# Performance work log

Hardware: AMD Instinct MI355X
Metric: run time of the kernel (lower is better)

The kernel has to match this reference:

```python
import jax, jax.numpy as jnp
import numpy as np

H = 256
NUM_LAYERS = 3
EPS = 1e-5


def _batchnorm(x, g, b):
    # training-mode BN over axis 0 (biased variance, as torch)
    m = x.mean(axis=0)
    v = x.var(axis=0)
    return (x - m) * jax.lax.rsqrt(v + EPS) * g + b


def _layernorm(x, g, b):
    m = x.mean(axis=-1, keepdims=True)
    v = x.var(axis=-1, keepdims=True)
    return (x - m) * jax.lax.rsqrt(v + EPS) * g + b


def setup_inputs() -> dict:
    key = jax.random.key(0)
    ks = iter(jax.random.split(key, 40))
    B, N = 8, 256
    s = 0.05
    inp = {
        "node_features": jax.random.normal(next(ks), (B, N, 6), jnp.float32),
        "edge_features": jax.random.normal(next(ks), (B, N, N, 15), jnp.float32),
        "temporal_features": jax.random.normal(next(ks), (B, N, N, 4), jnp.float32),
        "adjacency": jax.random.randint(next(ks), (N, N), 0, 2, jnp.int32),
        # node embedding + BN
        "emb_W": jax.random.normal(next(ks), (H, 6), jnp.float32) * s,
        "emb_b": jnp.zeros((H,), jnp.float32),
        "node_bn_g": jnp.ones((H,), jnp.float32),
        "node_bn_b": jnp.zeros((H,), jnp.float32),
        # message passing layers (stacked over layers)
        "msg_W": jax.random.normal(next(ks), (NUM_LAYERS, H, H + 3), jnp.float32) * s,
        "msg_b": jnp.zeros((NUM_LAYERS, H), jnp.float32),
        "upd_W": jax.random.normal(next(ks), (NUM_LAYERS, H, 2 * H), jnp.float32) * s,
        "upd_b": jnp.zeros((NUM_LAYERS, H), jnp.float32),
        "bn_g": jnp.ones((NUM_LAYERS, H), jnp.float32),
        "bn_b": jnp.zeros((NUM_LAYERS, H), jnp.float32),
        # flow predictor: 2H+3+4 -> 128 -> 64 -> 1
        "fp_W1": jax.random.normal(next(ks), (128, 2 * H + 7), jnp.float32) * s,
        "fp_b1": jnp.zeros((128,), jnp.float32),
        "fp_ln1_g": jnp.ones((128,), jnp.float32),
        "fp_ln1_b": jnp.zeros((128,), jnp.float32),
        "fp_W2": jax.random.normal(next(ks), (64, 128), jnp.float32) * s,
        "fp_b2": jnp.zeros((64,), jnp.float32),
        "fp_ln2_g": jnp.ones((64,), jnp.float32),
        "fp_ln2_b": jnp.zeros((64,), jnp.float32),
        "fp_W3": jax.random.normal(next(ks), (1, 64), jnp.float32) * s,
        "fp_b3": jnp.zeros((1,), jnp.float32),
    }
    return inp


def reference(node_features, edge_features, temporal_features, adjacency,
              emb_W, emb_b, node_bn_g, node_bn_b,
              msg_W, msg_b, upd_W, upd_b, bn_g, bn_b,
              fp_W1, fp_b1, fp_ln1_g, fp_ln1_b,
              fp_W2, fp_b2, fp_ln2_g, fp_ln2_b, fp_W3, fp_b3):
    B, N = node_features.shape[0], node_features.shape[1]
    # node embedding + BN + relu (dropout = identity at eval)
    emb = node_features @ emb_W.T + emb_b  # [B,N,H]
    emb = _batchnorm(emb.reshape(-1, H), node_bn_g, node_bn_b).reshape(B, N, H)
    emb = jax.nn.relu(emb)

    er = edge_features[..., -3:]  # [B,N,N,3], indexed er[:, i, j]
    maskf = (adjacency > 0).astype(emb.dtype)  # mask[j,i]: i is neighbor of j
    deg = maskf.sum(axis=1)  # [N]

    for l in range(NUM_LAYERS):
        Wn = msg_W[l][:, :H]   # [H,H] acting on source node embedding
        We = msg_W[l][:, H:]   # [H,3] acting on edge relation
        # messages[b,j] = sum_i mask[j,i] * (emb[b,i]@Wn.T + er[b,i,j]@We.T + b)
        m1 = jnp.einsum('ji,bio->bjo', maskf, emb @ Wn.T)
        er_sum = jnp.einsum('ji,bijk->bjk', maskf, er)  # [B,N,3]
        m2 = er_sum @ We.T
        messages = m1 + m2 + deg[None, :, None] * msg_b[l]
        upd_in = jnp.concatenate([emb, messages], axis=-1)  # [B,N,2H]
        updated = jax.nn.relu(upd_in @ upd_W[l].T + upd_b[l])
        updated = _batchnorm(updated.reshape(-1, H), bn_g[l], bn_b[l]).reshape(B, N, H)
        emb = updated + emb

    # flow predictor over all (i,j) pairs, input = [emb_i, emb_j, er_ij, t_ij]
    W1i = fp_W1[:, :H]
    W1j = fp_W1[:, H:2 * H]
    W1e = fp_W1[:, 2 * H:2 * H + 3]
    W1t = fp_W1[:, 2 * H + 3:]
    h = ((emb @ W1i.T)[:, :, None, :] + (emb @ W1j.T)[:, None, :, :]
         + er @ W1e.T + temporal_features @ W1t.T + fp_b1)  # [B,N,N,128]
    h = jax.nn.relu(_layernorm(h, fp_ln1_g, fp_ln1_b))
    h = jax.nn.relu(_layernorm(h @ fp_W2.T + fp_b2, fp_ln2_g, fp_ln2_b))  # [B,N,N,64]
    flows = jax.nn.relu((h @ fp_W3.T + fp_b3)[..., 0])  # [B,N,N]
    return flows
```

## Files before the change

### kernel.cpp

```cpp
#include <hip/hip_runtime.h>

#define NB 8
#define NN 256
#define HH 256
#define RR 2048
#define EPSV 1e-5f

typedef __attribute__((ext_vector_type(8))) short short8v;
typedef __attribute__((ext_vector_type(4))) float f32x4;

static __device__ __forceinline__ short f2bf(float f){
    unsigned u = __float_as_uint(f);
    unsigned r = (u + 0x7FFFu + ((u >> 16) & 1u)) >> 16;
    return (short)r;
}

static __device__ __forceinline__ float dpp_red16(float v){
    int t;
    t = __builtin_amdgcn_update_dpp(0, __float_as_int(v), 0xB1, 0xF, 0xF, true);
    v += __int_as_float(t);
    t = __builtin_amdgcn_update_dpp(0, __float_as_int(v), 0x4E, 0xF, 0xF, true);
    v += __int_as_float(t);
    t = __builtin_amdgcn_update_dpp(0, __float_as_int(v), 0x141, 0xF, 0xF, true);
    v += __int_as_float(t);
    t = __builtin_amdgcn_update_dpp(0, __float_as_int(v), 0x140, 0xF, 0xF, true);
    v += __int_as_float(t);
    return v;
}

__global__ __launch_bounds__(256) void k_emb(const float* __restrict__ nodef,
    const float* __restrict__ embW, const float* __restrict__ embb, float* __restrict__ out)
{
    int r = blockIdx.x, c = threadIdx.x;
    const float* nr = nodef + r*6;
    const float* w  = embW + c*6;
    float acc = embb[c];
    #pragma unroll
    for(int k=0;k<6;k++) acc += nr[k]*w[k];
    out[r*HH + c] = acc;
}

__global__ __launch_bounds__(256) void k_bnstat_partial(const float* __restrict__ x, float* __restrict__ part)
{
    int g = blockIdx.x, c = threadIdx.x;
    float s=0.f, q=0.f;
    #pragma unroll
    for(int rr=0; rr<32; rr++){
        float v = x[(g*32+rr)*HH + c];
        s += v; q += v*v;
    }
    part[g*512 + c]       = s;
    part[g*512 + 256 + c] = q;
}

__global__ __launch_bounds__(256) void k_bnstat_final(const float* __restrict__ part,
    const float* __restrict__ gam, const float* __restrict__ bet,
    float* __restrict__ scale, float* __restrict__ shift)
{
    int c = threadIdx.x;
    float s=0.f, q=0.f;
    for(int g=0; g<64; g++){ s += part[g*512+c]; q += part[g*512+256+c]; }
    float m  = s * (1.f/RR);
    float v  = q * (1.f/RR) - m*m;
    float sc = gam[c] * rsqrtf(v + EPSV);
    scale[c] = sc;
    shift[c] = bet[c] - m*sc;
}

__global__ __launch_bounds__(256) void k_bnapply_relu(const float* __restrict__ x,
    const float* __restrict__ scale, const float* __restrict__ shift, float* __restrict__ emb)
{
    int e = blockIdx.x*256 + threadIdx.x;
    int c = threadIdx.x;
    float v = x[e]*scale[c] + shift[c];
    emb[e] = v > 0.f ? v : 0.f;
}

__global__ __launch_bounds__(256) void k_bnapply_res(const float* __restrict__ x,
    const float* __restrict__ scale, const float* __restrict__ shift, float* __restrict__ emb)
{
    int e = blockIdx.x*256 + threadIdx.x;
    int c = threadIdx.x;
    emb[e] += x[e]*scale[c] + shift[c];
}

__global__ __launch_bounds__(256) void k_ersum_deg(const int* __restrict__ adj,
    const float* __restrict__ ef, float* __restrict__ ersum, float* __restrict__ degv)
{
    __shared__ float sd[4][256];
    int bid = blockIdx.x;
    int b = bid >> 8, j = bid & 255;
    int i = threadIdx.x;
    float mf = adj[j*NN + i] > 0 ? 1.f : 0.f;
    int base = ((b*NN + i)*NN + j)*15 + 12;
    sd[0][i] = mf * ef[base+0];
    sd[1][i] = mf * ef[base+1];
    sd[2][i] = mf * ef[base+2];
    sd[3][i] = mf;
    __syncthreads();
    for(int s=128; s>0; s>>=1){
        if(i < s){
            sd[0][i]+=sd[0][i+s]; sd[1][i]+=sd[1][i+s];
            sd[2][i]+=sd[2][i+s]; sd[3][i]+=sd[3][i+s];
        }
        __syncthreads();
    }
    if(i==0){
        ersum[(b*NN+j)*3+0] = sd[0][0];
        ersum[(b*NN+j)*3+1] = sd[1][0];
        ersum[(b*NN+j)*3+2] = sd[2][0];
        if(b==0) degv[j] = sd[3][0];
    }
}

__global__ __launch_bounds__(256) void k_mm(const float* __restrict__ A1, const float* __restrict__ A2,
    const float* __restrict__ W, int K, int ldw, int woff,
    const float* __restrict__ bias, int dorelu, float* __restrict__ C, int Co)
{
    __shared__ float As[32][20];
    __shared__ float Ws[64][20];
    int tid = threadIdx.x;
    int c0 = blockIdx.x*64, r0 = blockIdx.y*32;
    int tx = tid & 15, ty = tid >> 4;
    float acc[2][4] = {};
    for(int k0=0; k0<K; k0+=16){
        #pragma unroll
        for(int it=0; it<2; it++){
            int e = tid + it*256;
            int r = e >> 4, kk = e & 15;
            int k = k0 + kk;
            As[r][kk] = (k < 256) ? A1[(r0+r)*HH + k] : A2[(r0+r)*HH + (k-256)];
        }
        #pragma unroll
        for(int it=0; it<4; it++){
            int e = tid + it*256;
            int r = e >> 4, kk = e & 15;
            Ws[r][kk] = W[(c0+r)*ldw + woff + k0 + kk];
        }
        __syncthreads();
        #pragma unroll
        for(int kv=0; kv<4; kv++){
            float a4[2][4], w4[4][4];
            #pragma unroll
            for(int i=0;i<2;i++){
                float4 t1 = *reinterpret_cast<const float4*>(&As[ty*2+i][kv*4]);
                a4[i][0]=t1.x; a4[i][1]=t1.y; a4[i][2]=t1.z; a4[i][3]=t1.w;
            }
            #pragma unroll
            for(int i=0;i<4;i++){
                float4 t2 = *reinterpret_cast<const float4*>(&Ws[tx*4+i][kv*4]);
                w4[i][0]=t2.x; w4[i][1]=t2.y; w4[i][2]=t2.z; w4[i][3]=t2.w;
            }
            #pragma unroll
            for(int e=0;e<4;e++)
                #pragma unroll
                for(int i=0;i<2;i++)
                    #pragma unroll
                    for(int j=0;j<4;j++)
                        acc[i][j] += a4[i][e]*w4[j][e];
        }
        __syncthreads();
    }
    #pragma unroll
    for(int i=0;i<2;i++){
        int rg = r0 + ty*2 + i;
        #pragma unroll
        for(int j=0;j<4;j++){
            int cg = c0 + tx*4 + j;
            float v = acc[i][j];
            if(bias) v += bias[cg];
            if(dorelu) v = v > 0.f ? v : 0.f;
            C[rg*Co + cg] = v;
        }
    }
}

__global__ __launch_bounds__(256) void k_msg(const int* __restrict__ adj, const float* __restrict__ t,
    const float* __restrict__ ersum, const float* __restrict__ degv,
    const float* __restrict__ msgWl, const float* __restrict__ msgbl, float* __restrict__ msgs)
{
    __shared__ float As[32][20];
    __shared__ float Bs[64][20];
    int tid = threadIdx.x;
    int o0 = blockIdx.x*64, j0 = blockIdx.y*32, b = blockIdx.z;
    const float* tb = t + b*NN*HH;
    int tx = tid & 15, ty = tid >> 4;
    float acc[2][4] = {};
    for(int k0=0; k0<NN; k0+=16){
        #pragma unroll
        for(int it=0; it<2; it++){
            int e = tid + it*256;
            int r = e >> 4, kk = e & 15;
            As[r][kk] = adj[(j0+r)*NN + k0 + kk] > 0 ? 1.f : 0.f;
        }
        #pragma unroll
        for(int it=0; it<4; it++){
            int e = tid + it*256;
            int c = e & 63, k2 = e >> 6;
            Bs[c][k2] = tb[(k0+k2)*HH + o0 + c];
        }
        __syncthreads();
        #pragma unroll
        for(int kv=0; kv<4; kv++){
            float a4[2][4], w4[4][4];
            #pragma unroll
            for(int i=0;i<2;i++){
                float4 t1 = *reinterpret_cast<const float4*>(&As[ty*2+i][kv*4]);
                a4[i][0]=t1.x; a4[i][1]=t1.y; a4[i][2]=t1.z; a4[i][3]=t1.w;
            }
            #pragma unroll
            for(int i=0;i<4;i++){
                float4 t2 = *reinterpret_cast<const float4*>(&Bs[tx*4+i][kv*4]);
                w4[i][0]=t2.x; w4[i][1]=t2.y; w4[i][2]=t2.z; w4[i][3]=t2.w;
            }
            #pragma unroll
            for(int e=0;e<4;e++)
                #pragma unroll
                for(int i=0;i<2;i++)
                    #pragma unroll
                    for(int j=0;j<4;j++)
                        acc[i][j] += a4[i][e]*w4[j][e];
        }
        __syncthreads();
    }
    #pragma unroll
    for(int i=0;i<2;i++){
        int jg = j0 + ty*2 + i;
        const float* es = ersum + (b*NN + jg)*3;
        float dg = degv[jg];
        #pragma unroll
        for(int j=0;j<4;j++){
            int og = o0 + tx*4 + j;
            const float* we = msgWl + og*259 + 256;
            float v = acc[i][j] + es[0]*we[0] + es[1]*we[1] + es[2]*we[2] + dg*msgbl[og];
            msgs[(b*NN+jg)*HH + og] = v;
        }
    }
}

__global__ __launch_bounds__(256) void k_pack(const float* __restrict__ fpW2,
    const float* __restrict__ fpW1, unsigned short* __restrict__ w2bf, float* __restrict__ wext)
{
    int t = blockIdx.x*256 + threadIdx.x;
    if(t < 8192) w2bf[t] = (unsigned short)f2bf(fpW2[t]);
    if(t < 896){
        int p = t >> 7, o = t & 127;
        wext[p*128 + o] = fpW1[o*519 + 512 + p];
    }
}

__global__ __launch_bounds__(256) void k_fp2(
    const float* __restrict__ aW,
    const float* __restrict__ cW,
    const float* __restrict__ ef, const float* __restrict__ tfe,
    const float* __restrict__ wext,
    const float* __restrict__ gl1, const float* __restrict__ lb1,
    const unsigned short* __restrict__ w2bf,
    const float* __restrict__ fpb2,
    const float* __restrict__ g2, const float* __restrict__ lb2,
    const float* __restrict__ fpW3, const float* __restrict__ fpb3,
    float* __restrict__ out)
{
    __shared__ __align__(16) float wextS[896];
    __shared__ __align__(16) float g1S[128], lb1S[128];
    __shared__ __align__(16) float b2S[64], g2S[64], lb2S[64], w3S[64];

    int tid  = threadIdx.x;

    #pragma unroll
    for(int e=tid; e<896; e+=256) wextS[e] = wext[e];
    if(tid < 128){ g1S[tid] = gl1[tid]; lb1S[tid] = lb1[tid]; }
    else if(tid < 192){
        int p = tid - 128;
        b2S[p] = fpb2[p]; g2S[p] = g2[p]; lb2S[p] = lb2[p]; w3S[p] = fpW3[p];
    }
    __syncthreads();

    int w    = tid >> 6, lane = tid & 63;
    int x    = lane & 15, g = lane >> 4;
    int idx  = blockIdx.x;
    int jt   = idx & 3, ni = (idx >> 2) & 255, b = idx >> 10;
    int j0   = jt*64;
    int pos  = w*16 + x;
    int j    = j0 + pos;
    int eb   = (b*NN + ni)*NN + j;

    const float* ep = ef + eb*15 + 12;
    float er0 = ep[0], er1 = ep[1], er2 = ep[2];
    float4 tv = *(const float4*)(tfe + eb*4);

    const int obase = g*8;
    const float* arow = aW + (b*NN + ni)*128;
    const float* crow = cW + (b*NN + j)*128;

    float h[32];
    float s = 0.f, sq = 0.f;
    #pragma unroll
    for(int c=0;c<4;c++){
        const int o0 = c*32 + obase;
        const float4 a0 = *(const float4*)(arow + o0);
        const float4 a1 = *(const float4*)(arow + o0 + 4);
        const float4 c0v = *(const float4*)(crow + o0);
        const float4 c1v = *(const float4*)(crow + o0 + 4);
        float base[8] = {a0.x+c0v.x, a0.y+c0v.y, a0.z+c0v.z, a0.w+c0v.w,
                         a1.x+c1v.x, a1.y+c1v.y, a1.z+c1v.z, a1.w+c1v.w};
        #pragma unroll
        for(int p=0;p<7;p++){
            const float4 q0 = *(const float4*)(wextS + p*128 + o0);
            const float4 q1 = *(const float4*)(wextS + p*128 + o0 + 4);
            float coef = (p==0)?er0:(p==1)?er1:(p==2)?er2:(p==3)?tv.x:(p==4)?tv.y:(p==5)?tv.z:tv.w;
            base[0] += coef*q0.x; base[1] += coef*q0.y; base[2] += coef*q0.z; base[3] += coef*q0.w;
            base[4] += coef*q1.x; base[5] += coef*q1.y; base[6] += coef*q1.z; base[7] += coef*q1.w;
        }
        #pragma unroll
        for(int u=0;u<8;u++){ float v = base[u]; h[c*8+u] = v; s += v; sq += v*v; }
    }

    s  += __shfl_xor(s, 16);  s  += __shfl_xor(s, 32);
    sq += __shfl_xor(sq, 16); sq += __shfl_xor(sq, 32);
    float m   = s * (1.f/128.f);
    float var = sq * (1.f/128.f) - m*m;
    float rs  = rsqrtf(var + EPSV);

    short8v fa[4];
    #pragma unroll
    for(int c=0;c<4;c++){
        const int o0 = c*32 + obase;
        const float4 gg0 = *(const float4*)(g1S + o0);
        const float4 gg1 = *(const float4*)(g1S + o0 + 4);
        const float4 bb0 = *(const float4*)(lb1S + o0);
        const float4 bb1 = *(const float4*)(lb1S + o0 + 4);
        float gg[8] = {gg0.x,gg0.y,gg0.z,gg0.w, gg1.x,gg1.y,gg1.z,gg1.w};
        float bb[8] = {bb0.x,bb0.y,bb0.z,bb0.w, bb1.x,bb1.y,bb1.z,bb1.w};
        #pragma unroll
        for(int u=0;u<8;u++){
            float v = (h[c*8+u]-m)*rs*gg[u] + bb[u];
            v = v > 0.f ? v : 0.f;
            fa[c][u] = f2bf(v);
        }
    }

    f32x4 acc[4];
    #pragma unroll
    for(int n=0;n<4;n++){ acc[n].x=0.f; acc[n].y=0.f; acc[n].z=0.f; acc[n].w=0.f; }
    #pragma unroll
    for(int n=0;n<4;n++){
        #pragma unroll
        for(int c=0;c<4;c++){
            short8v bw = *(const short8v*)(w2bf + ((n*16 + x)*128 + c*32 + obase));
            acc[n] = __builtin_amdgcn_mfma_f32_16x16x32_bf16(fa[c], bw, acc[n], 0, 0, 0);
        }
    }

    float b2v[4], g2v[4], lb2v[4], w3v[4];
    #pragma unroll
    for(int n=0;n<4;n++){
        int p = n*16 + x;
        b2v[n] = b2S[p]; g2v[n] = g2S[p]; lb2v[n] = lb2S[p]; w3v[n] = w3S[p];
    }
    float b3 = fpb3[0];

    #pragma unroll
    for(int r=0;r<4;r++){
        float hv[4];
        float s2 = 0.f, q2 = 0.f;
        #pragma unroll
        for(int n=0;n<4;n++){
            float v = acc[n][r] + b2v[n];
            hv[n] = v; s2 += v; q2 += v*v;
        }
        s2 = dpp_red16(s2);
        q2 = dpp_red16(q2);
        float m2  = s2*(1.f/64.f);
        float v2  = q2*(1.f/64.f) - m2*m2;
        float rs2 = rsqrtf(v2 + EPSV);
        float fl = 0.f;
        #pragma unroll
        for(int n=0;n<4;n++){
            float v = (hv[n]-m2)*rs2*g2v[n] + lb2v[n];
            v = v > 0.f ? v : 0.f;
            fl += v * w3v[n];
        }
        fl = dpp_red16(fl);
        if(x == 0){
            float v = fl + b3;
            out[(b*NN + ni)*NN + j0 + w*16 + g*4 + r] = v > 0.f ? v : 0.f;
        }
    }
}

extern "C" void kernel_launch(void* const* d_in, const int* in_sizes, int n_in,
                              void* d_out, int out_size, void* d_ws, size_t ws_size,
                              hipStream_t stream) {
    const float* nodef = (const float*)d_in[0];
    const float* ef    = (const float*)d_in[1];
    const float* tfe   = (const float*)d_in[2];
    const int*   adj   = (const int*)d_in[3];
    const float* embW  = (const float*)d_in[4];
    const float* embb  = (const float*)d_in[5];
    const float* nbn_g = (const float*)d_in[6];
    const float* nbn_b = (const float*)d_in[7];
    const float* msgW  = (const float*)d_in[8];
    const float* msgb  = (const float*)d_in[9];
    const float* updW  = (const float*)d_in[10];
    const float* updb  = (const float*)d_in[11];
    const float* bng   = (const float*)d_in[12];
    const float* bnb   = (const float*)d_in[13];
    const float* fpW1  = (const float*)d_in[14];
    const float* fpb1  = (const float*)d_in[15];
    const float* g1    = (const float*)d_in[16];
    const float* lb1   = (const float*)d_in[17];
    const float* fpW2  = (const float*)d_in[18];
    const float* fpb2  = (const float*)d_in[19];
    const float* g2    = (const float*)d_in[20];
    const float* lb2   = (const float*)d_in[21];
    const float* fpW3  = (const float*)d_in[22];
    const float* fpb3  = (const float*)d_in[23];
    float* outp = (float*)d_out;

    float* ws    = (float*)d_ws;
    float* emb   = ws;
    float* buf1  = ws + 524288;
    float* msgs  = ws + 1048576;
    float* aW    = ws + 1572864;
    float* cW    = ws + 1835008;
    float* ersum = ws + 2097152;
    float* degv  = ws + 2103296;
    float* scale = ws + 2103552;
    float* shift = ws + 2103808;
    float* part  = ws + 2104064;
    unsigned short* w2bf = (unsigned short*)(ws + 2136832);
    float* wext  = ws + 2140928;

    k_pack<<<32, 256, 0, stream>>>(fpW2, fpW1, w2bf, wext);

    k_emb<<<RR, 256, 0, stream>>>(nodef, embW, embb, buf1);
    k_bnstat_partial<<<64, 256, 0, stream>>>(buf1, part);
    k_bnstat_final<<<1, 256, 0, stream>>>(part, nbn_g, nbn_b, scale, shift);
    k_bnapply_relu<<<RR, 256, 0, stream>>>(buf1, scale, shift, emb);

    k_ersum_deg<<<RR, 256, 0, stream>>>(adj, ef, ersum, degv);

    for(int l=0; l<3; l++){
        const float* msgWl = msgW + l*HH*259;
        const float* msgbl = msgb + l*HH;
        const float* updWl = updW + l*HH*512;
        const float* updbl = updb + l*HH;
        k_mm<<<dim3(4,64), 256, 0, stream>>>(emb, (const float*)nullptr, msgWl, 256, 259, 0,
                                             (const float*)nullptr, 0, buf1, 256);
        k_msg<<<dim3(4,8,8), 256, 0, stream>>>(adj, buf1, ersum, degv, msgWl, msgbl, msgs);
        k_mm<<<dim3(4,64), 256, 0, stream>>>(emb, msgs, updWl, 512, 512, 0,
                                             updbl, 1, buf1, 256);
        k_bnstat_partial<<<64, 256, 0, stream>>>(buf1, part);
        k_bnstat_final<<<1, 256, 0, stream>>>(part, bng + l*HH, bnb + l*HH, scale, shift);
        k_bnapply_res<<<RR, 256, 0, stream>>>(buf1, scale, shift, emb);
    }

    k_mm<<<dim3(2,64), 256, 0, stream>>>(emb, (const float*)nullptr, fpW1, 256, 519, 0,
                                         fpb1, 0, aW, 128);
    k_mm<<<dim3(2,64), 256, 0, stream>>>(emb, (const float*)nullptr, fpW1, 256, 519, 256,
                                         (const float*)nullptr, 0, cW, 128);

    k_fp2<<<NB*NN*4, 256, 0, stream>>>(aW, cW, ef, tfe, wext, g1, lb1,
                                       w2bf, fpb2, g2, lb2, fpW3, fpb3, outp);
}
```

Measured before the change: 450.0 us.

## Fuse embedding with BN stats and register-prefetch GEMM tiles with K=32

```diff
diff --git a/kernel.cpp b/kernel.cpp
--- a/kernel.cpp
+++ b/kernel.cpp
@@ -28,16 +28,29 @@
     return v;
 }
 
-__global__ __launch_bounds__(256) void k_emb(const float* __restrict__ nodef,
-    const float* __restrict__ embW, const float* __restrict__ embb, float* __restrict__ out)
-{
-    int r = blockIdx.x, c = threadIdx.x;
-    const float* nr = nodef + r*6;
-    const float* w  = embW + c*6;
-    float acc = embb[c];
-    #pragma unroll
-    for(int k=0;k<6;k++) acc += nr[k]*w[k];
-    out[r*HH + c] = acc;
+struct f3v { float x, y, z; };
+
+__global__ __launch_bounds__(256) void k_embstat(const float* __restrict__ nodef,
+    const float* __restrict__ embW, const float* __restrict__ embb,
+    float* __restrict__ buf1, float* __restrict__ part)
+{
+    int g = blockIdx.x, c = threadIdx.x;
+    float w[6];
+    #pragma unroll
+    for(int k=0;k<6;k++) w[k] = embW[c*6+k];
+    float bb = embb[c];
+    float s=0.f, q=0.f;
+    for(int rr=0; rr<32; rr++){
+        int r = g*32 + rr;
+        const float* nr = nodef + r*6;
+        float acc = bb;
+        #pragma unroll
+        for(int k=0;k<6;k++) acc += nr[k]*w[k];
+        buf1[r*HH + c] = acc;
+        s += acc; q += acc*acc;
+    }
+    part[g*512 + c]       = s;
+    part[g*512 + 256 + c] = q;
 }
 
 __global__ __launch_bounds__(256) void k_bnstat_partial(const float* __restrict__ x, float* __restrict__ part)
@@ -117,29 +130,40 @@
     const float* __restrict__ W, int K, int ldw, int woff,
     const float* __restrict__ bias, int dorelu, float* __restrict__ C, int Co)
 {
-    __shared__ float As[32][20];
-    __shared__ float Ws[64][20];
+    __shared__ float As[32][36];
+    __shared__ float Ws[64][36];
     int tid = threadIdx.x;
     int c0 = blockIdx.x*64, r0 = blockIdx.y*32;
     int tx = tid & 15, ty = tid >> 4;
+    int ar = tid >> 3,  ak = (tid & 7) * 4;
+    int wr = tid >> 2,  wk = (tid & 3) * 8;
     float acc[2][4] = {};
-    for(int k0=0; k0<K; k0+=16){
-        #pragma unroll
-        for(int it=0; it<2; it++){
-            int e = tid + it*256;
-            int r = e >> 4, kk = e & 15;
-            int k = k0 + kk;
-            As[r][kk] = (k < 256) ? A1[(r0+r)*HH + k] : A2[(r0+r)*HH + (k-256)];
-        }
-        #pragma unroll
-        for(int it=0; it<4; it++){
-            int e = tid + it*256;
-            int r = e >> 4, kk = e & 15;
-            Ws[r][kk] = W[(c0+r)*ldw + woff + k0 + kk];
-        }
+
+    float4 av; float wv[8];
+    {
+        int k = ak;
+        av = (k < 256 || !A2) ? *(const float4*)(A1 + (r0+ar)*HH + k)
+                              : *(const float4*)(A2 + (r0+ar)*HH + (k-256));
+        const float* wp = W + (c0+wr)*ldw + woff + wk;
+        #pragma unroll
+        for(int u=0;u<8;u++) wv[u] = wp[u];
+    }
+
+    for(int k0=0; k0<K; k0+=32){
+        *(float4*)&As[ar][ak] = av;
+        #pragma unroll
+        for(int u=0;u<8;u++) Ws[wr][wk+u] = wv[u];
         __syncthreads();
-        #pragma unroll
-        for(int kv=0; kv<4; kv++){
+        if(k0 + 32 < K){
+            int k = k0 + 32 + ak;
+            av = (k < 256) ? *(const float4*)(A1 + (r0+ar)*HH + k)
+                           : *(const float4*)(A2 + (r0+ar)*HH + (k-256));
+            const float* wp = W + (c0+wr)*ldw + woff + k0 + 32 + wk;
+            #pragma unroll
+            for(int u=0;u<8;u++) wv[u] = wp[u];
+        }
+        #pragma unroll
+        for(int kv=0; kv<8; kv++){
             float a4[2][4], w4[4][4];
             #pragma unroll
             for(int i=0;i<2;i++){
@@ -179,29 +203,58 @@
     const float* __restrict__ ersum, const float* __restrict__ degv,
     const float* __restrict__ msgWl, const float* __restrict__ msgbl, float* __restrict__ msgs)
 {
-    __shared__ float As[32][20];
-    __shared__ float Bs[64][20];
+    __shared__ float As[32][36];
+    __shared__ float Bs[64][36];
     int tid = threadIdx.x;
     int o0 = blockIdx.x*64, j0 = blockIdx.y*32, b = blockIdx.z;
     const float* tb = t + b*NN*HH;
     int tx = tid & 15, ty = tid >> 4;
     float acc[2][4] = {};
-    for(int k0=0; k0<NN; k0+=16){
-        #pragma unroll
-        for(int it=0; it<2; it++){
-            int e = tid + it*256;
-            int r = e >> 4, kk = e & 15;
-            As[r][kk] = adj[(j0+r)*NN + k0 + kk] > 0 ? 1.f : 0.f;
-        }
+
+    int a_pref[4]; float b_pref[8];
+    #pragma unroll
+    for(int it=0; it<4; it++){
+        int e = tid + it*256;
+        int r = e >> 5, kk = e & 31;
+        a_pref[it] = adj[(j0+r)*NN + kk];
+    }
+    #pragma unroll
+    for(int it=0; it<8; it++){
+        int e = tid + it*256;
+        int c = e & 63, k2 = e >> 6;
+        b_pref[it] = tb[k2*HH + o0 + c];
+    }
+
+    for(int k0=0; k0<NN; k0+=32){
         #pragma unroll
         for(int it=0; it<4; it++){
             int e = tid + it*256;
+            int r = e >> 5, kk = e & 31;
+            As[r][kk] = a_pref[it] > 0 ? 1.f : 0.f;
+        }
+        #pragma unroll
+        for(int it=0; it<8; it++){
+            int e = tid + it*256;
             int c = e & 63, k2 = e >> 6;
-            Bs[c][k2] = tb[(k0+k2)*HH + o0 + c];
+            Bs[c][k2] = b_pref[it];
         }
         __syncthreads();
-        #pragma unroll
-        for(int kv=0; kv<4; kv++){
+        if(k0 + 32 < NN){
+            #pragma unroll
+            for(int it=0; it<4; it++){
+                int e = tid + it*256;
+                int r = e >> 5, kk = e & 31;
+                a_pref[it] = adj[(j0+r)*NN + k0 + 32 + kk];
+            }
+            #pragma unroll
+            for(int it=0; it<8; it++){
+                int e = tid + it*256;
+                int c = e & 63, k2 = e >> 6;
+                b_pref[it] = tb[(k0 + 32 + k2)*HH + o0 + c];
+            }
+        }
+        #pragma unroll
+        for(int kv=0; kv<8; kv++){
             float a4[2][4], w4[4][4];
             #pragma unroll
             for(int i=0;i<2;i++){
@@ -285,8 +338,8 @@
     int j    = j0 + pos;
     int eb   = (b*NN + ni)*NN + j;
 
-    const float* ep = ef + eb*15 + 12;
-    float er0 = ep[0], er1 = ep[1], er2 = ep[2];
+    f3v e3 = *(const f3v*)(ef + eb*15 + 12);
+    float er0 = e3.x, er1 = e3.y, er2 = e3.z;
     float4 tv = *(const float4*)(tfe + eb*4);
 
     const int obase = g*8;
@@ -434,8 +487,7 @@
 
     k_pack<<<32, 256, 0, stream>>>(fpW2, fpW1, w2bf, wext);
 
-    k_emb<<<RR, 256, 0, stream>>>(nodef, embW, embb, buf1);
-    k_bnstat_partial<<<64, 256, 0, stream>>>(buf1, part);
+    k_embstat<<<64, 256, 0, stream>>>(nodef, embW, embb, buf1, part);
     k_bnstat_final<<<1, 256, 0, stream>>>(part, nbn_g, nbn_b, scale, shift);
     k_bnapply_relu<<<RR, 256, 0, stream>>>(buf1, scale, shift, emb);
 
```

After: 532.7 us. 18.4% more time.

## Fuse embedding with BN stats, stage aW row in LDS, switch MFMA to fp16

Applied to the files above, without the earlier changes.

```diff
diff --git a/kernel.cpp b/kernel.cpp
--- a/kernel.cpp
+++ b/kernel.cpp
@@ -6,14 +6,8 @@
 #define RR 2048
 #define EPSV 1e-5f
 
-typedef __attribute__((ext_vector_type(8))) short short8v;
+typedef __attribute__((ext_vector_type(8))) _Float16 half8v;
 typedef __attribute__((ext_vector_type(4))) float f32x4;
-
-static __device__ __forceinline__ short f2bf(float f){
-    unsigned u = __float_as_uint(f);
-    unsigned r = (u + 0x7FFFu + ((u >> 16) & 1u)) >> 16;
-    return (short)r;
-}
 
 static __device__ __forceinline__ float dpp_red16(float v){
     int t;
@@ -28,16 +22,29 @@
     return v;
 }
 
-__global__ __launch_bounds__(256) void k_emb(const float* __restrict__ nodef,
-    const float* __restrict__ embW, const float* __restrict__ embb, float* __restrict__ out)
-{
-    int r = blockIdx.x, c = threadIdx.x;
-    const float* nr = nodef + r*6;
-    const float* w  = embW + c*6;
-    float acc = embb[c];
-    #pragma unroll
-    for(int k=0;k<6;k++) acc += nr[k]*w[k];
-    out[r*HH + c] = acc;
+struct f3v { float x, y, z; };
+
+__global__ __launch_bounds__(256) void k_embstat(const float* __restrict__ nodef,
+    const float* __restrict__ embW, const float* __restrict__ embb,
+    float* __restrict__ buf1, float* __restrict__ part)
+{
+    int g = blockIdx.x, c = threadIdx.x;
+    float w[6];
+    #pragma unroll
+    for(int k=0;k<6;k++) w[k] = embW[c*6+k];
+    float bb = embb[c];
+    float s=0.f, q=0.f;
+    for(int rr=0; rr<32; rr++){
+        int r = g*32 + rr;
+        const float* nr = nodef + r*6;
+        float acc = bb;
+        #pragma unroll
+        for(int k=0;k<6;k++) acc += nr[k]*w[k];
+        buf1[r*HH + c] = acc;
+        s += acc; q += acc*acc;
+    }
+    part[g*512 + c]       = s;
+    part[g*512 + 256 + c] = q;
 }
 
 __global__ __launch_bounds__(256) void k_bnstat_partial(const float* __restrict__ x, float* __restrict__ part)
@@ -239,10 +246,13 @@
 }
 
 __global__ __launch_bounds__(256) void k_pack(const float* __restrict__ fpW2,
-    const float* __restrict__ fpW1, unsigned short* __restrict__ w2bf, float* __restrict__ wext)
+    const float* __restrict__ fpW1, unsigned short* __restrict__ w2hf, float* __restrict__ wext)
 {
     int t = blockIdx.x*256 + threadIdx.x;
-    if(t < 8192) w2bf[t] = (unsigned short)f2bf(fpW2[t]);
+    if(t < 8192){
+        _Float16 h = (_Float16)fpW2[t];
+        w2hf[t] = *reinterpret_cast<unsigned short*>(&h);
+    }
     if(t < 896){
         int p = t >> 7, o = t & 127;
         wext[p*128 + o] = fpW1[o*519 + 512 + p];
@@ -255,22 +265,26 @@
     const float* __restrict__ ef, const float* __restrict__ tfe,
     const float* __restrict__ wext,
     const float* __restrict__ gl1, const float* __restrict__ lb1,
-    const unsigned short* __restrict__ w2bf,
+    const unsigned short* __restrict__ w2hf,
     const float* __restrict__ fpb2,
     const float* __restrict__ g2, const float* __restrict__ lb2,
     const float* __restrict__ fpW3, const float* __restrict__ fpb3,
     float* __restrict__ out)
 {
     __shared__ __align__(16) float wextS[896];
-    __shared__ __align__(16) float g1S[128], lb1S[128];
+    __shared__ __align__(16) float g1S[128], lb1S[128], aWS[128];
     __shared__ __align__(16) float b2S[64], g2S[64], lb2S[64], w3S[64];
 
     int tid  = threadIdx.x;
+    int idx  = blockIdx.x;
+    int jt   = idx & 3, ni = (idx >> 2) & 255, b = idx >> 10;
 
     #pragma unroll
     for(int e=tid; e<896; e+=256) wextS[e] = wext[e];
-    if(tid < 128){ g1S[tid] = gl1[tid]; lb1S[tid] = lb1[tid]; }
-    else if(tid < 192){
+    if(tid < 128){
+        g1S[tid] = gl1[tid]; lb1S[tid] = lb1[tid];
+        aWS[tid] = aW[(b*NN + ni)*128 + tid];
+    } else if(tid < 192){
         int p = tid - 128;
         b2S[p] = fpb2[p]; g2S[p] = g2[p]; lb2S[p] = lb2[p]; w3S[p] = fpW3[p];
     }
@@ -278,19 +292,16 @@
 
     int w    = tid >> 6, lane = tid & 63;
     int x    = lane & 15, g = lane >> 4;
-    int idx  = blockIdx.x;
-    int jt   = idx & 3, ni = (idx >> 2) & 255, b = idx >> 10;
     int j0   = jt*64;
     int pos  = w*16 + x;
     int j    = j0 + pos;
     int eb   = (b*NN + ni)*NN + j;
 
-    const float* ep = ef + eb*15 + 12;
-    float er0 = ep[0], er1 = ep[1], er2 = ep[2];
+    f3v e3 = *(const f3v*)(ef + eb*15 + 12);
+    float er0 = e3.x, er1 = e3.y, er2 = e3.z;
     float4 tv = *(const float4*)(tfe + eb*4);
 
     const int obase = g*8;
-    const float* arow = aW + (b*NN + ni)*128;
     const float* crow = cW + (b*NN + j)*128;
 
     float h[32];
@@ -298,8 +309,8 @@
     #pragma unroll
     for(int c=0;c<4;c++){
         const int o0 = c*32 + obase;
-        const float4 a0 = *(const float4*)(arow + o0);
-        const float4 a1 = *(const float4*)(arow + o0 + 4);
+        const float4 a0 = *(const float4*)(aWS + o0);
+        const float4 a1 = *(const float4*)(aWS + o0 + 4);
         const float4 c0v = *(const float4*)(crow + o0);
         const float4 c1v = *(const float4*)(crow + o0 + 4);
         float base[8] = {a0.x+c0v.x, a0.y+c0v.y, a0.z+c0v.z, a0.w+c0v.w,
@@ -322,7 +333,7 @@
     float var = sq * (1.f/128.f) - m*m;
     float rs  = rsqrtf(var + EPSV);
 
-    short8v fa[4];
+    half8v fa[4];
     #pragma unroll
     for(int c=0;c<4;c++){
         const int o0 = c*32 + obase;
@@ -336,7 +347,7 @@
         for(int u=0;u<8;u++){
             float v = (h[c*8+u]-m)*rs*gg[u] + bb[u];
             v = v > 0.f ? v : 0.f;
-            fa[c][u] = f2bf(v);
+            fa[c][u] = (_Float16)v;
         }
     }
 
@@ -347,8 +358,8 @@
     for(int n=0;n<4;n++){
         #pragma unroll
         for(int c=0;c<4;c++){
-            short8v bw = *(const short8v*)(w2bf + ((n*16 + x)*128 + c*32 + obase));
-            acc[n] = __builtin_amdgcn_mfma_f32_16x16x32_bf16(fa[c], bw, acc[n], 0, 0, 0);
+            half8v bw = *(const half8v*)(w2hf + ((n*16 + x)*128 + c*32 + obase));
+            acc[n] = __builtin_amdgcn_mfma_f32_16x16x32_f16(fa[c], bw, acc[n], 0, 0, 0);
         }
     }
 
@@ -429,13 +440,12 @@
     float* scale = ws + 2103552;
     float* shift = ws + 2103808;
     float* part  = ws + 2104064;
-    unsigned short* w2bf = (unsigned short*)(ws + 2136832);
+    unsigned short* w2hf = (unsigned short*)(ws + 2136832);
     float* wext  = ws + 2140928;
 
-    k_pack<<<32, 256, 0, stream>>>(fpW2, fpW1, w2bf, wext);
-
-    k_emb<<<RR, 256, 0, stream>>>(nodef, embW, embb, buf1);
-    k_bnstat_partial<<<64, 256, 0, stream>>>(buf1, part);
+    k_pack<<<32, 256, 0, stream>>>(fpW2, fpW1, w2hf, wext);
+
+    k_embstat<<<64, 256, 0, stream>>>(nodef, embW, embb, buf1, part);
     k_bnstat_final<<<1, 256, 0, stream>>>(part, nbn_g, nbn_b, scale, shift);
     k_bnapply_relu<<<RR, 256, 0, stream>>>(buf1, scale, shift, emb);
 
@@ -462,5 +472,5 @@
                                          (const float*)nullptr, 0, cW, 128);
 
     k_fp2<<<NB*NN*4, 256, 0, stream>>>(aW, cW, ef, tfe, wext, g1, lb1,
-                                       w2bf, fpb2, g2, lb2, fpW3, fpb3, outp);
-}
+                                       w2hf, fpb2, g2, lb2, fpW3, fpb3, outp);
+}
```

Measured after the change: 443.6 us (median of 2 runs). About the same (-1.4%).
